# Kernel tuning notes

Measured on AMD Instinct MI355X. Metric: run time of the kernel, lower is better.

Reference implementation:

```python
import jax, jax.numpy as jnp
import numpy as np

EPS = 1e-08
K = 3  # kernel size


def _conv_same_per_sample(xi, wi):
    # xi: [Cin,H,W], wi: [Cout,Cin,K,K] -> [Cout,H,W]
    out = jax.lax.conv_general_dilated(
        xi[None],  # [1,Cin,H,W]
        wi,
        window_strides=(1, 1),
        padding=((K // 2, K // 2), (K // 2, K // 2)),
        dimension_numbers=("NCHW", "OIHW", "NCHW"),
    )
    return out[0]


def setup_inputs() -> dict:
    key = jax.random.key(0)
    ks = jax.random.split(key, 6)
    B, Cin, Cout, S, H, W = 16, 256, 256, 512, 64, 64
    x = jax.random.normal(ks[0], (B, Cin, H, W), dtype=jnp.float32)
    y = jax.random.normal(ks[1], (B, S), dtype=jnp.float32)
    weights = jax.random.normal(ks[2], (Cout, Cin, K, K), dtype=jnp.float32)
    bias = jnp.zeros((Cout,), dtype=jnp.float32)
    # nn.Linear(style_channels, in_channels)
    lim = 1.0 / np.sqrt(S)
    style_w = jax.random.uniform(ks[3], (Cin, S), jnp.float32, -lim, lim)
    style_b = jax.random.uniform(ks[4], (Cin,), jnp.float32, -lim, lim)
    return {"x": x, "y": y, "weights": weights, "bias": bias,
            "style_w": style_w, "style_b": style_b}


def reference(x, y, weights, bias, style_w, style_b):
    # style: [B, Cin]
    style = y @ style_w.T + style_b
    # modulate: [B, Cout, Cin, K, K]
    w_mod = weights[None] * style[:, None, :, None, None]
    # demodulate over (Cin, K, K)
    w_std = jnp.sqrt(jnp.sum(w_mod * w_mod, axis=(2, 3, 4), keepdims=True) + EPS)
    w_demod = w_mod / w_std
    # per-sample conv (equivalent to groups=batch grouped conv)
    out = jax.vmap(_conv_same_per_sample)(x, w_demod)  # [B,Cout,H,W]
    return out + bias[None, :, None, None]
```

## Files before the change

kernel.cpp:

```cpp
#include <hip/hip_runtime.h>

typedef __bf16 bf16;
typedef __bf16 bf16x8 __attribute__((ext_vector_type(8)));
typedef float f32x4 __attribute__((ext_vector_type(4)));

#define EPS 1e-8f

constexpr int B = 16, CI = 256, CO = 256, S = 512, H = 64, W = 64;
constexpr int PH = 66;
constexpr int TAPS = 9;

constexpr size_t WS_WD    = 0;
constexpr size_t WS_XPAD  = 1179648;
constexpr size_t WS_STYLE = WS_XPAD + (size_t)B*PH*32*PH*16;
constexpr size_t WS_WSQT  = WS_STYLE + 16384;
constexpr size_t WS_INV   = WS_WSQT + 262144;

__global__ void prep1_kernel(const float* __restrict__ y,
                             const float* __restrict__ sw,
                             const float* __restrict__ sb,
                             const float* __restrict__ wts,
                             bf16x8* __restrict__ wd,
                             float* __restrict__ wsqT,
                             float* __restrict__ style) {
    __shared__ float t[8 * 289];
    int i = blockIdx.x;
    if (i < 256) {
        int cb = i & 31;
        int ib = i >> 5;
        const float* src = wts + ((size_t)cb * 8) * (CI * TAPS) + ib * 32 * TAPS;
        for (int e = threadIdx.x; e < 8 * 288; e += 256) {
            int col = e / 288, idx = e - col * 288;
            t[col * 289 + idx] = src[(size_t)col * (CI * TAPS) + idx];
        }
        __syncthreads();
        for (int c = threadIdx.x; c < 288; c += 256) {
            int co_l = c & 7, ci8_l = (c >> 3) & 3, tap = c >> 5;
            bf16x8 v;
#pragma unroll
            for (int j = 0; j < 8; ++j) v[j] = (bf16)t[co_l * 289 + (ci8_l * 8 + j) * 9 + tap];
            wd[((size_t)tap * 32 + ib * 4 + ci8_l) * CO + cb * 8 + co_l] = v;
        }
        int c = threadIdx.x;
        int co_l = c & 7, ci_l = c >> 3;
        float s = 0.f;
#pragma unroll
        for (int tap = 0; tap < 9; ++tap) {
            float w = t[co_l * 289 + ci_l * 9 + tap];
            s += w * w;
        }
        wsqT[((size_t)(ib * 32 + ci_l)) * CO + cb * 8 + co_l] = s;
    } else {
        int i2 = i - 256;
        int b = i2 >> 6;
        int c = (i2 & 63) * 4 + (threadIdx.x >> 6);
        int lane = threadIdx.x & 63;
        const float* yr = y + (size_t)b * S;
        const float* wr = sw + (size_t)c * S;
        float acc = 0.f;
#pragma unroll
        for (int k = 0; k < 8; ++k) acc += yr[lane + k * 64] * wr[lane + k * 64];
        for (int off = 32; off; off >>= 1) acc += __shfl_down(acc, off, 64);
        if (lane == 0) style[b * CI + c] = acc + sb[c];
    }
}

__global__ void prep2_kernel(const float* __restrict__ x,
                             const float* __restrict__ style,
                             const float* __restrict__ wsqT,
                             bf16x8* __restrict__ xp,
                             float* __restrict__ invstd) {
    __shared__ float st2[256];
    int i = blockIdx.x;
    if (i < 8192) {
        int b = i >> 9, rem = i & 511;
        int ci8 = rem & 31;
        int row = ((rem >> 5) << 2) + (threadIdx.x >> 6);
        int col = threadIdx.x & 63;
        const float* xb = x + (((size_t)b * CI + ci8 * 8) * H + row) * W + col;
        const float* st = style + b * CI + ci8 * 8;
        bf16x8 v;
#pragma unroll
        for (int j = 0; j < 8; ++j) v[j] = (bf16)(xb[(size_t)j * H * W] * st[j]);
        xp[(((size_t)b * PH + row + 1) * 32 + ci8) * PH + col + 1] = v;
        return;
    }
    if (i < 8448) {
        int bi = i - 8192;
        int b = bi >> 4, part = bi & 15;
        bf16x8 z;
#pragma unroll
        for (int j = 0; j < 8; ++j) z[j] = (bf16)0.f;
        for (int t = threadIdx.x; t < 520; t += 256) {
            int idx = part * 520 + t;
            int row, ci8, col;
            if (idx < 4224) {
                int rowsel = idx / 2112;
                int rem = idx - rowsel * 2112;
                row = rowsel ? (PH - 1) : 0;
                ci8 = rem / 66;
                col = rem - ci8 * 66;
            } else {
                int j2 = idx - 4224;
                int colsel = j2 >> 11;
                int rem = j2 & 2047;
                row = 1 + (rem >> 5);
                ci8 = rem & 31;
                col = colsel ? (PH - 1) : 0;
            }
            xp[(((size_t)b * PH + row) * 32 + ci8) * PH + col] = z;
        }
        return;
    }
    int b = i - 8448, co = threadIdx.x;
    float s = style[b * CI + co];
    st2[co] = s * s;
    __syncthreads();
    float a0 = 0.f, a1 = 0.f, a2 = 0.f, a3 = 0.f;
    float a4 = 0.f, a5 = 0.f, a6 = 0.f, a7 = 0.f;
    for (int ci = 0; ci < CI; ci += 8) {
        a0 += wsqT[(size_t)(ci + 0) * CO + co] * st2[ci + 0];
        a1 += wsqT[(size_t)(ci + 1) * CO + co] * st2[ci + 1];
        a2 += wsqT[(size_t)(ci + 2) * CO + co] * st2[ci + 2];
        a3 += wsqT[(size_t)(ci + 3) * CO + co] * st2[ci + 3];
        a4 += wsqT[(size_t)(ci + 4) * CO + co] * st2[ci + 4];
        a5 += wsqT[(size_t)(ci + 5) * CO + co] * st2[ci + 5];
        a6 += wsqT[(size_t)(ci + 6) * CO + co] * st2[ci + 6];
        a7 += wsqT[(size_t)(ci + 7) * CO + co] * st2[ci + 7];
    }
    float acc = ((a0 + a1) + (a2 + a3)) + ((a4 + a5) + (a6 + a7));
    invstd[b * CO + co] = rsqrtf(acc + EPS);
}

#define LOAD_TAP(c8_, kh_, kw_, av_, bv_)                                         \
    {                                                                             \
        const bf16x8* wq_ = wbase + ((size_t)((kh_)*3 + (kw_)) * 32 + (c8_)) * CO;\
        const bf16x8* xq_ = xbase + ((size_t)(kh_) * 32 * PH + (size_t)(c8_) * PH + (kw_)); \
        _Pragma("unroll") for (int a_ = 0; a_ < 4; ++a_) (av_)[a_] = wq_[a_ * 16];\
        _Pragma("unroll") for (int jr_ = 0; jr_ < 2; ++jr_)                       \
            _Pragma("unroll") for (int jc_ = 0; jc_ < 4; ++jc_)                   \
                (bv_)[jr_ * 4 + jc_] = xq_[(size_t)jr_ * 32 * PH + jc_ * 16];     \
    }

#define MFMA_STEP(av_, bv_)                                                       \
    __builtin_amdgcn_s_setprio(1);                                                \
    _Pragma("unroll") for (int a_ = 0; a_ < 4; ++a_)                              \
        _Pragma("unroll") for (int j_ = 0; j_ < 8; ++j_)                          \
            acc[a_][j_] = __builtin_amdgcn_mfma_f32_16x16x32_bf16(                \
                (av_)[a_], (bv_)[j_], acc[a_][j_], 0, 0, 0);                      \
    __builtin_amdgcn_s_setprio(0);

__global__ __launch_bounds__(256, 2) void conv_kernel(
                            const bf16x8* __restrict__ wd,
                            const bf16x8* __restrict__ xp,
                            const float* __restrict__ bias,
                            const float* __restrict__ invstd,
                            float* __restrict__ out) {
    int i = blockIdx.x;
    int xcd = i & 7, t = i >> 3;
    int b = xcd * 2 + (t >> 5);
    int rest = t & 31;
    int cotile = rest & 1, rowquad = rest >> 1;
    int tid = threadIdx.x;
    int wave = tid >> 6, lane = tid & 63;
    int co_half = wave & 1, sp_half = wave >> 1;
    int r0 = rowquad * 4 + sp_half * 2;
    int co_base = cotile * 128 + co_half * 64;
    int lm = lane & 15, lk = lane >> 4;

    f32x4 acc[4][8] = {};

    const bf16x8* xpb = xp + (size_t)b * PH * 32 * PH;
    const bf16x8* wbase = wd + (size_t)lk * CO + co_base + lm;
    const bf16x8* xbase = xpb + ((size_t)r0 * 32 + lk) * PH + lm;

    bf16x8 av0[4], bv0[8], av1[4], bv1[8];

    LOAD_TAP(0, 0, 0, av0, bv0);

#pragma unroll 1
    for (int c8a = 0; c8a < 32; c8a += 8) {
#pragma unroll
        for (int v = 0; v < 18; ++v) {
            const int ntap = (v + 1) % 9;
            const int nkh = ntap / 3, nkw = ntap % 3;
            int nc8 = (v == 17) ? ((c8a + 8) & 31)
                                : (c8a + ((v + 1) / 9) * 4);
            if ((v & 1) == 0) {
                LOAD_TAP(nc8, nkh, nkw, av1, bv1);
                __builtin_amdgcn_sched_barrier(0);
                MFMA_STEP(av0, bv0);
            } else {
                LOAD_TAP(nc8, nkh, nkw, av0, bv0);
                __builtin_amdgcn_sched_barrier(0);
                MFMA_STEP(av1, bv1);
            }
        }
    }

#pragma unroll
    for (int a = 0; a < 4; ++a) {
#pragma unroll
        for (int g = 0; g < 4; ++g) {
            int co = co_base + a * 16 + lk * 4 + g;
            float sc = invstd[b * CO + co];
            float bvl = bias[co];
#pragma unroll
            for (int jr = 0; jr < 2; ++jr) {
                size_t o = (((size_t)b * CO + co) * H + r0 + jr) * W;
#pragma unroll
                for (int jc = 0; jc < 4; ++jc)
                    out[o + jc * 16 + lm] = acc[a][jr * 4 + jc][g] * sc + bvl;
            }
        }
    }
}

extern "C" void kernel_launch(void* const* d_in, const int* in_sizes, int n_in,
                              void* d_out, int out_size, void* d_ws, size_t ws_size,
                              hipStream_t stream) {
    const float* x    = (const float*)d_in[0];
    const float* y    = (const float*)d_in[1];
    const float* wts  = (const float*)d_in[2];
    const float* bias = (const float*)d_in[3];
    const float* sw   = (const float*)d_in[4];
    const float* sb   = (const float*)d_in[5];
    float* out = (float*)d_out;

    char* ws = (char*)d_ws;
    bf16x8* wd    = (bf16x8*)(ws + WS_WD);
    bf16x8* xpad  = (bf16x8*)(ws + WS_XPAD);
    float* style  = (float*)(ws + WS_STYLE);
    float* wsqT   = (float*)(ws + WS_WSQT);
    float* invstd = (float*)(ws + WS_INV);

    prep1_kernel<<<dim3(1280), dim3(256), 0, stream>>>(y, sw, sb, wts, wd, wsqT, style);
    prep2_kernel<<<dim3(8464), dim3(256), 0, stream>>>(x, style, wsqT, xpad, invstd);
    conv_kernel<<<dim3(512), dim3(256), 0, stream>>>(wd, xpad, bias, invstd, out);
}
```

Measured before the change: 191.8 us.

## Fuse two prep kernels into one launch, recomputing style per block

Merges the two preprocessing kernels into a single launch. The x-modulation blocks now compute their eight needed style values locally, and the invstd blocks compute the full style vector and squared-weight sums themselves, which removes the style and wsqT intermediates and the dependency between launches. It also adds XCD-aware block-to-batch mapping and nontemporal loads of x. The cost is redundant style dot products in every x block (8192 blocks each reading y and 8 rows of style_w) and a serial per-thread 2304-element weight reduction in 16 blocks, which may form a tail.

```diff
diff --git a/kernel.cpp b/kernel.cpp
--- a/kernel.cpp
+++ b/kernel.cpp
@@ -12,87 +12,117 @@
 
 constexpr size_t WS_WD    = 0;
 constexpr size_t WS_XPAD  = 1179648;
-constexpr size_t WS_STYLE = WS_XPAD + (size_t)B*PH*32*PH*16;
-constexpr size_t WS_WSQT  = WS_STYLE + 16384;
-constexpr size_t WS_INV   = WS_WSQT + 262144;
-
-__global__ void prep1_kernel(const float* __restrict__ y,
-                             const float* __restrict__ sw,
-                             const float* __restrict__ sb,
-                             const float* __restrict__ wts,
-                             bf16x8* __restrict__ wd,
-                             float* __restrict__ wsqT,
-                             float* __restrict__ style) {
+constexpr size_t WS_INV   = WS_XPAD + (size_t)B*PH*32*PH*16;
+
+__global__ __launch_bounds__(256) void prep_kernel(
+        const float* __restrict__ x,
+        const float* __restrict__ y,
+        const float* __restrict__ wts,
+        const float* __restrict__ sw,
+        const float* __restrict__ sb,
+        bf16x8* __restrict__ wd,
+        bf16x8* __restrict__ xp,
+        float* __restrict__ invstd) {
     __shared__ float t[8 * 289];
     int i = blockIdx.x;
+    int tid = threadIdx.x;
+
     if (i < 256) {
         int cb = i & 31;
         int ib = i >> 5;
         const float* src = wts + ((size_t)cb * 8) * (CI * TAPS) + ib * 32 * TAPS;
-        for (int e = threadIdx.x; e < 8 * 288; e += 256) {
+        for (int e = tid; e < 8 * 288; e += 256) {
             int col = e / 288, idx = e - col * 288;
             t[col * 289 + idx] = src[(size_t)col * (CI * TAPS) + idx];
         }
         __syncthreads();
-        for (int c = threadIdx.x; c < 288; c += 256) {
+        for (int c = tid; c < 288; c += 256) {
             int co_l = c & 7, ci8_l = (c >> 3) & 3, tap = c >> 5;
             bf16x8 v;
 #pragma unroll
             for (int j = 0; j < 8; ++j) v[j] = (bf16)t[co_l * 289 + (ci8_l * 8 + j) * 9 + tap];
             wd[((size_t)tap * 32 + ib * 4 + ci8_l) * CO + cb * 8 + co_l] = v;
         }
-        int c = threadIdx.x;
-        int co_l = c & 7, ci_l = c >> 3;
-        float s = 0.f;
-#pragma unroll
-        for (int tap = 0; tap < 9; ++tap) {
-            float w = t[co_l * 289 + ci_l * 9 + tap];
-            s += w * w;
-        }
-        wsqT[((size_t)(ib * 32 + ci_l)) * CO + cb * 8 + co_l] = s;
-    } else {
-        int i2 = i - 256;
-        int b = i2 >> 6;
-        int c = (i2 & 63) * 4 + (threadIdx.x >> 6);
-        int lane = threadIdx.x & 63;
+        return;
+    }
+    if (i < 272) {
+        int idx = i - 256;
+        int b = (idx & 7) * 2 + (idx >> 3);
+        int co = tid;
         const float* yr = y + (size_t)b * S;
-        const float* wr = sw + (size_t)c * S;
+        const float* wr = sw + (size_t)co * S;
+        float sacc = 0.f;
+#pragma unroll 4
+        for (int k = 0; k < S; k += 4) {
+            f32x4 yv = *(const f32x4*)(yr + k);
+            f32x4 wv = *(const f32x4*)(wr + k);
+            sacc += yv[0] * wv[0] + yv[1] * wv[1] + yv[2] * wv[2] + yv[3] * wv[3];
+        }
+        float stv = sacc + sb[co];
+        t[co] = stv * stv;
+        __syncthreads();
+        const float* wrow = wts + (size_t)co * (CI * TAPS);
         float acc = 0.f;
-#pragma unroll
-        for (int k = 0; k < 8; ++k) acc += yr[lane + k * 64] * wr[lane + k * 64];
-        for (int off = 32; off; off >>= 1) acc += __shfl_down(acc, off, 64);
-        if (lane == 0) style[b * CI + c] = acc + sb[c];
-    }
-}
-
-__global__ void prep2_kernel(const float* __restrict__ x,
-                             const float* __restrict__ style,
-                             const float* __restrict__ wsqT,
-                             bf16x8* __restrict__ xp,
-                             float* __restrict__ invstd) {
-    __shared__ float st2[256];
-    int i = blockIdx.x;
-    if (i < 8192) {
-        int b = i >> 9, rem = i & 511;
-        int ci8 = rem & 31;
-        int row = ((rem >> 5) << 2) + (threadIdx.x >> 6);
-        int col = threadIdx.x & 63;
+#pragma unroll 1
+        for (int ci = 0; ci < CI; ci += 4) {
+            f32x4 p[9];
+#pragma unroll
+            for (int v4 = 0; v4 < 9; ++v4)
+                p[v4] = *(const f32x4*)(wrow + ci * 9 + v4 * 4);
+#pragma unroll
+            for (int cc = 0; cc < 4; ++cc) {
+                float ws = 0.f;
+#pragma unroll
+                for (int tp = 0; tp < 9; ++tp) {
+                    int e = cc * 9 + tp;
+                    float wv2 = p[e >> 2][e & 3];
+                    ws += wv2 * wv2;
+                }
+                acc += ws * t[ci + cc];
+            }
+        }
+        invstd[b * CO + co] = rsqrtf(acc + EPS);
+        return;
+    }
+    if (i < 8464) {
+        int u = i - 272;
+        int xcd = u & 7, q = u >> 3;
+        int b = xcd * 2 + (q >> 9);
+        int w = q & 511;
+        int ci8 = w & 31, rowgrp = w >> 5;
+        int row = rowgrp * 4 + (tid >> 6), col = tid & 63;
+        int g = tid >> 5, gl = tid & 31;
+        {
+            const float* yr = y + (size_t)b * S;
+            const float* wr = sw + (size_t)(ci8 * 8 + g) * S;
+            float sacc = 0.f;
+#pragma unroll
+            for (int k2 = 0; k2 < 16; ++k2) sacc += yr[gl + k2 * 32] * wr[gl + k2 * 32];
+#pragma unroll
+            for (int off = 16; off; off >>= 1) sacc += __shfl_down(sacc, off, 32);
+            if (gl == 0) t[g] = sacc + sb[ci8 * 8 + g];
+        }
+        __syncthreads();
+        float st_l[8];
+#pragma unroll
+        for (int j = 0; j < 8; ++j) st_l[j] = t[j];
         const float* xb = x + (((size_t)b * CI + ci8 * 8) * H + row) * W + col;
-        const float* st = style + b * CI + ci8 * 8;
         bf16x8 v;
 #pragma unroll
-        for (int j = 0; j < 8; ++j) v[j] = (bf16)(xb[(size_t)j * H * W] * st[j]);
+        for (int jj = 0; jj < 8; ++jj)
+            v[jj] = (bf16)(__builtin_nontemporal_load(xb + (size_t)jj * H * W) * st_l[jj]);
         xp[(((size_t)b * PH + row + 1) * 32 + ci8) * PH + col + 1] = v;
         return;
     }
-    if (i < 8448) {
-        int bi = i - 8192;
-        int b = bi >> 4, part = bi & 15;
+    {
+        int v2 = i - 8464;
+        int xcd = v2 & 7, j = v2 >> 3;
+        int b = xcd * 2 + (j >> 4), part = j & 15;
         bf16x8 z;
 #pragma unroll
-        for (int j = 0; j < 8; ++j) z[j] = (bf16)0.f;
-        for (int t = threadIdx.x; t < 520; t += 256) {
-            int idx = part * 520 + t;
+        for (int jj = 0; jj < 8; ++jj) z[jj] = (bf16)0.f;
+        for (int tt = tid; tt < 520; tt += 256) {
+            int idx = part * 520 + tt;
             int row, ci8, col;
             if (idx < 4224) {
                 int rowsel = idx / 2112;
@@ -110,26 +140,7 @@
             }
             xp[(((size_t)b * PH + row) * 32 + ci8) * PH + col] = z;
         }
-        return;
-    }
-    int b = i - 8448, co = threadIdx.x;
-    float s = style[b * CI + co];
-    st2[co] = s * s;
-    __syncthreads();
-    float a0 = 0.f, a1 = 0.f, a2 = 0.f, a3 = 0.f;
-    float a4 = 0.f, a5 = 0.f, a6 = 0.f, a7 = 0.f;
-    for (int ci = 0; ci < CI; ci += 8) {
-        a0 += wsqT[(size_t)(ci + 0) * CO + co] * st2[ci + 0];
-        a1 += wsqT[(size_t)(ci + 1) * CO + co] * st2[ci + 1];
-        a2 += wsqT[(size_t)(ci + 2) * CO + co] * st2[ci + 2];
-        a3 += wsqT[(size_t)(ci + 3) * CO + co] * st2[ci + 3];
-        a4 += wsqT[(size_t)(ci + 4) * CO + co] * st2[ci + 4];
-        a5 += wsqT[(size_t)(ci + 5) * CO + co] * st2[ci + 5];
-        a6 += wsqT[(size_t)(ci + 6) * CO + co] * st2[ci + 6];
-        a7 += wsqT[(size_t)(ci + 7) * CO + co] * st2[ci + 7];
-    }
-    float acc = ((a0 + a1) + (a2 + a3)) + ((a4 + a5) + (a6 + a7));
-    invstd[b * CO + co] = rsqrtf(acc + EPS);
+    }
 }
 
 #define LOAD_TAP(c8_, kh_, kw_, av_, bv_)                                         \
@@ -157,9 +168,9 @@
                             const float* __restrict__ invstd,
                             float* __restrict__ out) {
     int i = blockIdx.x;
-    int xcd = i & 7, t = i >> 3;
-    int b = xcd * 2 + (t >> 5);
-    int rest = t & 31;
+    int xcd = i & 7, tq = i >> 3;
+    int b = xcd * 2 + (tq >> 5);
+    int rest = tq & 31;
     int cotile = rest & 1, rowquad = rest >> 1;
     int tid = threadIdx.x;
     int wave = tid >> 6, lane = tid & 63;
@@ -230,11 +241,8 @@
     char* ws = (char*)d_ws;
     bf16x8* wd    = (bf16x8*)(ws + WS_WD);
     bf16x8* xpad  = (bf16x8*)(ws + WS_XPAD);
-    float* style  = (float*)(ws + WS_STYLE);
-    float* wsqT   = (float*)(ws + WS_WSQT);
     float* invstd = (float*)(ws + WS_INV);
 
-    prep1_kernel<<<dim3(1280), dim3(256), 0, stream>>>(y, sw, sb, wts, wd, wsqT, style);
-    prep2_kernel<<<dim3(8464), dim3(256), 0, stream>>>(x, style, wsqT, xpad, invstd);
+    prep_kernel<<<dim3(8720), dim3(256), 0, stream>>>(x, y, wts, sw, sb, wd, xpad, invstd);
     conv_kernel<<<dim3(512), dim3(256), 0, stream>>>(wd, xpad, bias, invstd, out);
 }
```

Result: slower. 261.2 us (+36.2%).
